# Kernel optimization log

Hardware: AMD Instinct MI355X
Metric: run time of the kernel (lower is better)

The kernel has to match this reference:

```python
import jax, jax.numpy as jnp
import numpy as np

EPS = 1.1920929e-07  # torch RMSNorm default eps = finfo(float32).eps

def rmsnorm(x, w):
    return x * jax.lax.rsqrt(jnp.mean(x * x, axis=-1, keepdims=True) + EPS) * w

def setup_inputs() -> dict:
    key = jax.random.key(0)
    ks = jax.random.split(key, 12)
    D, H, SC, ST = 1024, 16, 64, 16
    B, T = 2, 2048
    s = 0.02
    return {
        "x": jax.random.normal(ks[0], (B, T, D), jnp.float32),
        "qkv_w": jax.random.normal(ks[1], (3 * D, D), jnp.float32) * s,
        "o_w": jax.random.normal(ks[2], (D, D), jnp.float32) * s,
        "norm1_w": jnp.ones((D,), jnp.float32),
        "norm2_w": jnp.ones((D,), jnp.float32),
        "in_w": jax.random.normal(ks[3], (SC, D), jnp.float32) * s,
        "out_w": jax.random.normal(ks[4], (D, SC), jnp.float32) * s,  # zeros in torch init; randn for nontrivial baseline
        "A_log": jax.random.normal(ks[5], (SC, ST), jnp.float32) * 0.1,
        "Bp_w": jax.random.normal(ks[6], (ST, SC), jnp.float32) * s,
        "Cp_w": jax.random.normal(ks[7], (ST, SC), jnp.float32) * s,
        "dt_w": jax.random.normal(ks[8], (SC, SC), jnp.float32) * s,
        "dt_b": jnp.full((SC,), -3.0, jnp.float32),
        "gate_w": jax.random.normal(ks[9], (SC, D), jnp.float32) * s,
    }

def selective_scan(h, in_w, out_w, A_log, Bp_w, Cp_w, dt_w, dt_b, gate_w):
    B, T, D = h.shape
    SC, ST = A_log.shape
    z = h @ in_w.T                      # [B,T,SC]
    gate = jax.nn.silu(h @ gate_w.T)    # [B,T,SC]
    A = -jnp.exp(A_log)                 # [SC,ST]
    Bi = z @ Bp_w.T                     # [B,T,ST]
    Ci = z @ Cp_w.T                     # [B,T,ST]
    dt = jax.nn.softplus(z @ dt_w.T + dt_b)  # [B,T,SC]
    A_bar = 1.0 + dt[..., None] * A     # [B,T,SC,ST]

    def step(state, inp):
        a_bar, dtz_t, b_t, c_t = inp    # [B,SC,ST],[B,SC],[B,ST],[B,ST]
        state = a_bar * state + dtz_t[:, :, None] * b_t[:, None, :]
        y = jnp.sum(state * c_t[:, None, :], axis=-1)  # [B,SC]
        return state, y

    init = jnp.zeros((B, SC, ST), h.dtype)
    xs = (jnp.swapaxes(A_bar, 0, 1), jnp.swapaxes(dt * z, 0, 1),
          jnp.swapaxes(Bi, 0, 1), jnp.swapaxes(Ci, 0, 1))
    _, ys = jax.lax.scan(step, init, xs)      # [T,B,SC]
    y = jnp.swapaxes(ys, 0, 1) * gate         # [B,T,SC]
    return y @ out_w.T                        # [B,T,D]

def reference(x, qkv_w, o_w, norm1_w, norm2_w, in_w, out_w, A_log, Bp_w, Cp_w, dt_w, dt_b, gate_w):
    B, T, D = x.shape
    H = 16
    hd = D // H
    h = rmsnorm(x, norm1_w)
    qkv = (h @ qkv_w.T).reshape(B, T, 3, H, hd)
    qkv = jnp.transpose(qkv, (2, 0, 3, 1, 4))  # [3,B,H,T,hd]
    q, k, v = qkv[0], qkv[1], qkv[2]
    attn = jnp.einsum('bhqd,bhkd->bhqk', q, k) / np.sqrt(hd).astype(np.float32)
    mask = jnp.tril(jnp.ones((T, T), bool))
    attn = jnp.where(mask, attn, -jnp.inf)
    attn = jax.nn.softmax(attn, axis=-1)
    out = jnp.einsum('bhqk,bhkd->bhqd', attn, v)
    out = jnp.transpose(out, (0, 2, 1, 3)).reshape(B, T, D)
    x = x + out @ o_w.T
    h2 = rmsnorm(x, norm2_w)
    x = x + selective_scan(h2, in_w, out_w, A_log, Bp_w, Cp_w, dt_w, dt_b, gate_w)
    return x
```

## Files before the change

### kernel.cpp

```cpp
#include <hip/hip_runtime.h>
#include <hip/hip_bf16.h>
#include <math.h>

typedef __hip_bfloat16 bf16;
typedef __attribute__((ext_vector_type(4))) float v_f32x4;
typedef __attribute__((ext_vector_type(4))) unsigned short v_u16x4;
typedef __attribute__((ext_vector_type(8))) unsigned short v_u16x8;
typedef __attribute__((ext_vector_type(8))) __bf16 v_bf16x8;

#define NB 2
#define NT 2048
#define ND 1024
#define NH 16
#define NSC 64
#define NST 16
#define NM (NB*NT)
#define RMS_EPS 1.1920929e-07f
#define NCHUNK 32
#define CLEN 64

__device__ inline float b2f(unsigned short u) {
  union { unsigned int i; float f; } v; v.i = ((unsigned int)u) << 16; return v.f;
}
__device__ inline unsigned short f2b(float f) {
  union { float f; unsigned int i; } v; v.f = f;
  unsigned int r = (v.i + 0x7FFF + ((v.i >> 16) & 1)) >> 16;
  return (unsigned short)r;
}

__device__ inline void gl_lds16(const bf16* g, bf16* l) {
  __builtin_amdgcn_global_load_lds((__attribute__((address_space(1))) void*)g,
                                   (__attribute__((address_space(3))) void*)l,
                                   16, 0, 0);
}

__global__ __launch_bounds__(256) void cvt_all_kernel(
    const float* __restrict__ qkv_w, const float* __restrict__ o_w,
    const float* __restrict__ out_w, const float* __restrict__ in_w,
    const float* __restrict__ gate_w, const float* __restrict__ dt_w,
    const float* __restrict__ Bp_w, const float* __restrict__ Cp_w,
    bf16* __restrict__ qkvw_b, bf16* __restrict__ ow_b, bf16* __restrict__ outw_b,
    bf16* __restrict__ W1, bf16* __restrict__ W2) {
  const int blk = blockIdx.x, t = threadIdx.x;
  const float* src; bf16* dst; int base;
  if (blk < 3072)      { src = qkv_w;  dst = qkvw_b;      base = blk; }
  else if (blk < 4096) { src = o_w;    dst = ow_b;        base = blk - 3072; }
  else if (blk < 4160) { src = out_w;  dst = outw_b;      base = blk - 4096; }
  else if (blk < 4224) { src = in_w;   dst = W1;          base = blk - 4160; }
  else if (blk < 4288) { src = gate_w; dst = W1 + 65536;  base = blk - 4224; }
  else if (blk < 4292) { src = dt_w;   dst = W2;          base = blk - 4288; }
  else if (blk == 4292){ src = Bp_w;   dst = W2 + 4096;   base = 0; }
  else if (blk == 4293){ src = Cp_w;   dst = W2 + 5120;   base = 0; }
  else {
    v_u16x8 z;
    #pragma unroll
    for (int i = 0; i < 8; i++) z[i] = 0;
    *(v_u16x8*)(W2 + 6144 + t * 8) = z;
    return;
  }
  int i = base * 256 + t;
  v_f32x4 v = ((const v_f32x4*)src)[i];
  v_u16x4 o;
  o[0] = f2b(v[0]); o[1] = f2b(v[1]); o[2] = f2b(v[2]); o[3] = f2b(v[3]);
  ((v_u16x4*)dst)[i] = o;
}

__global__ __launch_bounds__(256) void rmsnorm_kernel(
    const float* __restrict__ x, const float* __restrict__ w, bf16* __restrict__ out) {
  const int row = blockIdx.x;
  const int t = threadIdx.x;
  v_f32x4 xv = *(const v_f32x4*)(x + (size_t)row * ND + t * 4);
  float s = xv[0]*xv[0] + xv[1]*xv[1] + xv[2]*xv[2] + xv[3]*xv[3];
  #pragma unroll
  for (int off = 32; off; off >>= 1) s += __shfl_xor(s, off, 64);
  __shared__ float red[4];
  __shared__ float scale_s;
  if ((t & 63) == 0) red[t >> 6] = s;
  __syncthreads();
  if (t == 0) {
    float tot = red[0] + red[1] + red[2] + red[3];
    scale_s = rsqrtf(tot * (1.0f / ND) + RMS_EPS);
  }
  __syncthreads();
  float sc = scale_s;
  v_f32x4 wv = *(const v_f32x4*)(w + t * 4);
  unsigned short* orow = (unsigned short*)out + (size_t)row * ND + t * 4;
  v_u16x4 o;
  o[0] = f2b(xv[0] * sc * wv[0]);
  o[1] = f2b(xv[1] * sc * wv[1]);
  o[2] = f2b(xv[2] * sc * wv[2]);
  o[3] = f2b(xv[3] * sc * wv[3]);
  *(v_u16x4*)orow = o;
}

template <bool RES, bool OUTF32>
__global__ __launch_bounds__(256) void gemm_bt_kernel(
    const bf16* __restrict__ A, const bf16* __restrict__ Bw,
    const float* __restrict__ res, void* __restrict__ Cout, int N, int K, int lda) {
  __shared__ alignas(16) bf16 As[128 * 32];
  __shared__ alignas(16) bf16 Bs[128 * 32];
  const int tid = threadIdx.x;
  const int wid = tid >> 6;
  const int lane = tid & 63;
  const int c = lane & 15;
  const int quad = lane >> 4;
  const int m0 = blockIdx.y * 128;
  const int n0 = blockIdx.x * 128;
  const int wm = (wid >> 1) * 64;
  const int wn = (wid & 1) * 64;
  const int srow = tid >> 2;
  const int schunk = tid & 3;

  const bf16* Ap0 = A + (size_t)(m0 + srow) * lda + schunk * 8;
  const bf16* Ap1 = Ap0 + (size_t)64 * lda;
  const bf16* Bp0 = Bw + (size_t)(n0 + srow) * K + schunk * 8;
  const bf16* Bp1 = Bp0 + (size_t)64 * K;
  bf16* AsW0 = As + wid * 512;
  bf16* AsW1 = As + 2048 + wid * 512;
  bf16* BsW0 = Bs + wid * 512;
  bf16* BsW1 = Bs + 2048 + wid * 512;

  v_f32x4 acc[4][4];
  #pragma unroll
  for (int i = 0; i < 4; i++)
    #pragma unroll
    for (int j = 0; j < 4; j++)
      #pragma unroll
      for (int r = 0; r < 4; r++) acc[i][j][r] = 0.0f;

  const int nk = K >> 5;
  for (int kt = 0; kt < nk; kt++) {
    gl_lds16(Ap0 + kt * 32, AsW0);
    gl_lds16(Ap1 + kt * 32, AsW1);
    gl_lds16(Bp0 + kt * 32, BsW0);
    gl_lds16(Bp1 + kt * 32, BsW1);
    __syncthreads();
    v_bf16x8 af[4], bfw[4];
    #pragma unroll
    for (int i = 0; i < 4; i++)
      af[i] = *(const v_bf16x8*)&As[(wm + i * 16 + c) * 32 + quad * 8];
    #pragma unroll
    for (int j = 0; j < 4; j++)
      bfw[j] = *(const v_bf16x8*)&Bs[(wn + j * 16 + c) * 32 + quad * 8];
    #pragma unroll
    for (int i = 0; i < 4; i++)
      #pragma unroll
      for (int j = 0; j < 4; j++)
        acc[i][j] = __builtin_amdgcn_mfma_f32_16x16x32_bf16(af[i], bfw[j], acc[i][j], 0, 0, 0);
    __syncthreads();
  }

  #pragma unroll
  for (int i = 0; i < 4; i++)
    #pragma unroll
    for (int j = 0; j < 4; j++)
      #pragma unroll
      for (int r = 0; r < 4; r++) {
        int rg = m0 + wm + i * 16 + quad * 4 + r;
        int cg = n0 + wn + j * 16 + c;
        size_t idx = (size_t)rg * N + cg;
        float v = acc[i][j][r];
        if (RES) v += res[idx];
        if (OUTF32) ((float*)Cout)[idx] = v;
        else ((bf16*)Cout)[idx] = __float2bfloat16(v);
      }
}

template <bool RES, bool OUTF32>
__global__ __launch_bounds__(256) void gemm_bt64_kernel(
    const bf16* __restrict__ A, const bf16* __restrict__ Bw,
    const float* __restrict__ res, void* __restrict__ Cout, int N, int K, int lda) {
  __shared__ alignas(16) bf16 As[64 * 32];
  __shared__ alignas(16) bf16 Bs[128 * 32];
  const int tid = threadIdx.x;
  const int wid = tid >> 6;
  const int lane = tid & 63;
  const int c = lane & 15;
  const int quad = lane >> 4;
  const int m0 = blockIdx.y * 64;
  const int n0 = blockIdx.x * 128;
  const int wm = (wid & 1) * 32;
  const int wn = (wid >> 1) * 64;
  const int srow = tid >> 2;
  const int schunk = tid & 3;

  const bf16* Ap = A + (size_t)(m0 + srow) * lda + schunk * 8;
  const bf16* Bp0 = Bw + (size_t)(n0 + srow) * K + schunk * 8;
  const bf16* Bp1 = Bp0 + (size_t)64 * K;
  bf16* AsW  = As + wid * 512;
  bf16* BsW0 = Bs + wid * 512;
  bf16* BsW1 = Bs + 2048 + wid * 512;

  v_f32x4 acc[2][4];
  #pragma unroll
  for (int i = 0; i < 2; i++)
    #pragma unroll
    for (int j = 0; j < 4; j++)
      #pragma unroll
      for (int r = 0; r < 4; r++) acc[i][j][r] = 0.0f;

  const int nk = K >> 5;
  for (int kt = 0; kt < nk; kt++) {
    gl_lds16(Ap + kt * 32, AsW);
    gl_lds16(Bp0 + kt * 32, BsW0);
    gl_lds16(Bp1 + kt * 32, BsW1);
    __syncthreads();
    v_bf16x8 af[2], bfw[4];
    #pragma unroll
    for (int i = 0; i < 2; i++)
      af[i] = *(const v_bf16x8*)&As[(wm + i * 16 + c) * 32 + quad * 8];
    #pragma unroll
    for (int j = 0; j < 4; j++)
      bfw[j] = *(const v_bf16x8*)&Bs[(wn + j * 16 + c) * 32 + quad * 8];
    #pragma unroll
    for (int i = 0; i < 2; i++)
      #pragma unroll
      for (int j = 0; j < 4; j++)
        acc[i][j] = __builtin_amdgcn_mfma_f32_16x16x32_bf16(af[i], bfw[j], acc[i][j], 0, 0, 0);
    __syncthreads();
  }

  #pragma unroll
  for (int i = 0; i < 2; i++)
    #pragma unroll
    for (int j = 0; j < 4; j++)
      #pragma unroll
      for (int r = 0; r < 4; r++) {
        int rg = m0 + wm + i * 16 + quad * 4 + r;
        int cg = n0 + wn + j * 16 + c;
        size_t idx = (size_t)rg * N + cg;
        float v = acc[i][j][r];
        if (RES) v += res[idx];
        if (OUTF32) ((float*)Cout)[idx] = v;
        else ((bf16*)Cout)[idx] = __float2bfloat16(v);
      }
}

template <bool OUTF32>
__global__ __launch_bounds__(256) void gemm_skinny_kernel(
    const bf16* __restrict__ A, const bf16* __restrict__ Bw,
    void* __restrict__ Cout, int K, int lda) {
  __shared__ alignas(16) bf16 As[16 * 32];
  __shared__ alignas(16) bf16 Bs[128 * 32];
  const int tid = threadIdx.x;
  const int w = tid >> 6;
  const int lane = tid & 63;
  const int c = lane & 15;
  const int quad = lane >> 4;
  const int m0 = blockIdx.x * 16;
  const int lrow = lane >> 2, lchunk = lane & 3;

  const bf16* ApL = A + (size_t)(m0 + lrow) * lda + lchunk * 8;
  const bf16* BpL0 = Bw + (size_t)(w * 16 + lrow) * K + lchunk * 8;
  const bf16* BpL1 = Bw + (size_t)(64 + w * 16 + lrow) * K + lchunk * 8;
  bf16* BsW0 = Bs + w * 512;
  bf16* BsW1 = Bs + 2048 + w * 512;

  v_f32x4 acc[2];
  #pragma unroll
  for (int j = 0; j < 2; j++)
    #pragma unroll
    for (int r = 0; r < 4; r++) acc[j][r] = 0.0f;

  const int nk = K >> 5;
  for (int kt = 0; kt < nk; kt++) {
    if (w == 0) gl_lds16(ApL + kt * 32, As);
    gl_lds16(BpL0 + kt * 32, BsW0);
    gl_lds16(BpL1 + kt * 32, BsW1);
    __syncthreads();
    v_bf16x8 af = *(const v_bf16x8*)&As[c * 32 + quad * 8];
    #pragma unroll
    for (int j = 0; j < 2; j++) {
      v_bf16x8 bfw = *(const v_bf16x8*)&Bs[(w * 32 + j * 16 + c) * 32 + quad * 8];
      acc[j] = __builtin_amdgcn_mfma_f32_16x16x32_bf16(af, bfw, acc[j], 0, 0, 0);
    }
    __syncthreads();
  }

  #pragma unroll
  for (int j = 0; j < 2; j++)
    #pragma unroll
    for (int r = 0; r < 4; r++) {
      size_t idx = (size_t)(m0 + quad * 4 + r) * 128 + w * 32 + j * 16 + c;
      if (OUTF32) ((float*)Cout)[idx] = acc[j][r];
      else ((bf16*)Cout)[idx] = __float2bfloat16(acc[j][r]);
    }
}

__global__ __launch_bounds__(256) void vtrans_kernel(const bf16* __restrict__ qkv,
                                                     bf16* __restrict__ VtG) {
  __shared__ alignas(16) bf16 Vs[64 * 72];
  const int tid = threadIdx.x;
  const int t0 = blockIdx.x * 64;
  const int bh = blockIdx.y;
  const int b = bh >> 4, h = bh & 15;
  const int srow = tid >> 2, schunk = tid & 3;
  {
    const bf16* src = qkv + (size_t)(b * NT + t0 + srow) * 3072 + 2048 + h * 64 + schunk * 16;
    *(v_u16x8*)&Vs[srow * 72 + schunk * 16] = *(const v_u16x8*)src;
    *(v_u16x8*)&Vs[srow * 72 + schunk * 16 + 8] = *(const v_u16x8*)(src + 8);
  }
  __syncthreads();
  const unsigned short* Vsu = (const unsigned short*)Vs;
  v_u16x8 a, bvec;
  #pragma unroll
  for (int i = 0; i < 8; i++) a[i] = Vsu[(schunk * 16 + i) * 72 + srow];
  #pragma unroll
  for (int i = 0; i < 8; i++) bvec[i] = Vsu[(schunk * 16 + 8 + i) * 72 + srow];
  bf16* dst = VtG + (size_t)(bh * 64 + srow) * NT + t0 + schunk * 16;
  *(v_u16x8*)dst = a;
  *(v_u16x8*)(dst + 8) = bvec;
}

__global__ __launch_bounds__(256) void attn_kernel(const bf16* __restrict__ qkv,
                                                   const bf16* __restrict__ VtG,
                                                   bf16* __restrict__ out) {
  __shared__ alignas(16) bf16 Qs[128 * 72];
  __shared__ alignas(16) bf16 Ks[64 * 72];
  __shared__ alignas(16) bf16 Vt[64 * 72];
  __shared__ alignas(16) bf16 Ps[128 * 72];
  const int tid = threadIdx.x;
  const int w = tid >> 6;
  const int lane = tid & 63;
  const int c = lane & 15;
  const int quad = lane >> 4;
  const int id = blockIdx.x;
  const int bh = id & 31;
  const int j5 = id >> 5;
  const int qt2 = (j5 & 8) ? (15 - (j5 & 7)) : (j5 & 7);
  const int b = bh >> 4;
  const int h = bh & 15;
  const int srow = tid >> 2;
  const int schunk = tid & 3;
  const int qbase = qt2 * 128;

  #pragma unroll
  for (int g = 0; g < 2; g++) {
    const bf16* src = qkv + (size_t)(b * NT + qbase + g * 64 + srow) * 3072 + h * 64 + schunk * 16;
    *(v_u16x8*)&Qs[(g * 64 + srow) * 72 + schunk * 16] = *(const v_u16x8*)src;
    *(v_u16x8*)&Qs[(g * 64 + srow) * 72 + schunk * 16 + 8] = *(const v_u16x8*)(src + 8);
  }
  __syncthreads();
  v_bf16x8 aq[2][2];
  #pragma unroll
  for (int g = 0; g < 2; g++) {
    aq[g][0] = *(const v_bf16x8*)&Qs[(g * 64 + w * 16 + c) * 72 + quad * 8];
    aq[g][1] = *(const v_bf16x8*)&Qs[(g * 64 + w * 16 + c) * 72 + 32 + quad * 8];
  }

  float l_part[2][4];
  v_f32x4 o[2][4];
  #pragma unroll
  for (int g = 0; g < 2; g++)
    #pragma unroll
    for (int r = 0; r < 4; r++) l_part[g][r] = 0.0f;
  #pragma unroll
  for (int g = 0; g < 2; g++)
    #pragma unroll
    for (int j = 0; j < 4; j++)
      #pragma unroll
      for (int r = 0; r < 4; r++) o[g][j][r] = 0.0f;

  const int ktmax = 2 * qt2 + 1;
  for (int kt = 0; kt <= ktmax; kt++) {
    {
      const bf16* ksrc = qkv + (size_t)(b * NT + kt * 64 + srow) * 3072 + 1024 + h * 64 + schunk * 16;
      *(v_u16x8*)&Ks[srow * 72 + schunk * 16] = *(const v_u16x8*)ksrc;
      *(v_u16x8*)&Ks[srow * 72 + schunk * 16 + 8] = *(const v_u16x8*)(ksrc + 8);
      const bf16* vsrc = VtG + (size_t)(bh * 64 + srow) * NT + kt * 64 + schunk * 16;
      *(v_u16x8*)&Vt[srow * 72 + schunk * 16] = *(const v_u16x8*)vsrc;
      *(v_u16x8*)&Vt[srow * 72 + schunk * 16 + 8] = *(const v_u16x8*)(vsrc + 8);
    }
    __syncthreads();

    #pragma unroll
    for (int g = 0; g < 2; g++) {
      const int ktd = 2 * qt2 + g;
      if (kt <= ktd) {
        const bool diag = (kt == ktd);
        #pragma unroll
        for (int j4 = 0; j4 < 4; j4++) {
          v_bf16x8 bk0 = *(const v_bf16x8*)&Ks[(j4 * 16 + c) * 72 + quad * 8];
          v_bf16x8 bk1 = *(const v_bf16x8*)&Ks[(j4 * 16 + c) * 72 + 32 + quad * 8];
          v_f32x4 z;
          #pragma unroll
          for (int r = 0; r < 4; r++) z[r] = 0.0f;
          z = __builtin_amdgcn_mfma_f32_16x16x32_bf16(aq[g][0], bk0, z, 0, 0, 0);
          z = __builtin_amdgcn_mfma_f32_16x16x32_bf16(aq[g][1], bk1, z, 0, 0, 0);
          #pragma unroll
          for (int r = 0; r < 4; r++) {
            float p = __expf(z[r] * 0.125f);
            if (diag && (j4 * 16 + c) > (w * 16 + quad * 4 + r)) p = 0.0f;
            l_part[g][r] += p;
            Ps[(g * 64 + w * 16 + quad * 4 + r) * 72 + j4 * 16 + c] = __float2bfloat16(p);
          }
        }
        #pragma unroll
        for (int ks = 0; ks < 2; ks++) {
          v_bf16x8 ap = *(const v_bf16x8*)&Ps[(g * 64 + w * 16 + c) * 72 + ks * 32 + quad * 8];
          #pragma unroll
          for (int jn = 0; jn < 4; jn++) {
            v_bf16x8 bv = *(const v_bf16x8*)&Vt[(jn * 16 + c) * 72 + ks * 32 + quad * 8];
            o[g][jn] = __builtin_amdgcn_mfma_f32_16x16x32_bf16(ap, bv, o[g][jn], 0, 0, 0);
          }
        }
      }
    }
    __syncthreads();
  }

  #pragma unroll
  for (int g = 0; g < 2; g++)
    #pragma unroll
    for (int r = 0; r < 4; r++) {
      float l = l_part[g][r];
      l += __shfl_xor(l, 1, 64);
      l += __shfl_xor(l, 2, 64);
      l += __shfl_xor(l, 4, 64);
      l += __shfl_xor(l, 8, 64);
      l_part[g][r] = l;
    }

  #pragma unroll
  for (int g = 0; g < 2; g++)
    #pragma unroll
    for (int jn = 0; jn < 4; jn++)
      #pragma unroll
      for (int r = 0; r < 4; r++) {
        int qg = qbase + g * 64 + w * 16 + quad * 4 + r;
        out[(size_t)(b * NT + qg) * ND + h * 64 + jn * 16 + c] =
            __float2bfloat16(o[g][jn][r] / l_part[g][r]);
      }
}

__global__ __launch_bounds__(256) void scanprep_kernel(
    const bf16* __restrict__ zg, const float* __restrict__ P2, const float* __restrict__ dt_b,
    float* __restrict__ dt_a, float* __restrict__ dtz_a, float* __restrict__ gate_a) {
  const int row = blockIdx.x * 4 + (threadIdx.x >> 6);
  const int c = threadIdx.x & 63;
  const unsigned short* zgu = (const unsigned short*)zg;
  float z = b2f(zgu[(size_t)row * 128 + c]);
  float g = b2f(zgu[(size_t)row * 128 + 64 + c]);
  float a = P2[(size_t)row * 128 + c] + dt_b[c];
  float dt = (a > 20.0f) ? a : log1pf(__expf(a));
  dt_a[(size_t)row * NSC + c] = dt;
  dtz_a[(size_t)row * NSC + c] = dt * z;
  gate_a[(size_t)row * NSC + c] = g / (1.0f + __expf(-g));
}

__global__ __launch_bounds__(256) void scanA_kernel(
    const float* __restrict__ dt_a, const float* __restrict__ dtz_a,
    const float* __restrict__ P2, const float* __restrict__ A_log,
    float* __restrict__ Pbuf, float* __restrict__ Sbuf) {
  __shared__ float dtS[CLEN * 16], dtzS[CLEN * 16], biS[CLEN * 16];
  const int k = blockIdx.x, scg = blockIdx.y, b = blockIdx.z;
  const int tid = threadIdx.x;
  const int t0 = k * CLEN;
  {
    int r = tid >> 2, c4 = (tid & 3) * 4;
    *(v_f32x4*)&dtS[r * 16 + c4]  = *(const v_f32x4*)&dt_a[(size_t)(b * NT + t0 + r) * NSC + scg * 16 + c4];
    *(v_f32x4*)&dtzS[r * 16 + c4] = *(const v_f32x4*)&dtz_a[(size_t)(b * NT + t0 + r) * NSC + scg * 16 + c4];
    *(v_f32x4*)&biS[r * 16 + c4]  = *(const v_f32x4*)&P2[(size_t)(b * NT + t0 + r) * 128 + 64 + c4];
  }
  __syncthreads();
  const int st = tid & 15, scl = tid >> 4;
  const float A = -__expf(A_log[(scg * 16 + scl) * NST + st]);
  float P = 1.0f, s = 0.0f;
  #pragma unroll
  for (int t = 0; t < CLEN; t++) {
    float a = fmaf(dtS[t * 16 + scl], A, 1.0f);
    float u = dtzS[t * 16 + scl] * biS[t * 16 + st];
    P *= a;
    s = fmaf(a, s, u);
  }
  size_t idx = (size_t)(b * NCHUNK + k) * 1024 + scg * 256 + tid;
  Pbuf[idx] = P;
  Sbuf[idx] = s;
}

__global__ __launch_bounds__(1024) void scanB_kernel(
    const float* __restrict__ Pbuf, const float* __restrict__ Sbuf,
    float* __restrict__ init) {
  const int b = blockIdx.x;
  const int tid = threadIdx.x;
  float P[NCHUNK], S[NCHUNK];
  #pragma unroll
  for (int kk = 0; kk < NCHUNK; kk++) {
    size_t idx = (size_t)(b * NCHUNK + kk) * 1024 + tid;
    P[kk] = Pbuf[idx];
    S[kk] = Sbuf[idx];
  }
  float s = 0.0f;
  #pragma unroll
  for (int kk = 0; kk < NCHUNK; kk++) {
    init[(size_t)(b * NCHUNK + kk) * 1024 + tid] = s;
    s = fmaf(P[kk], s, S[kk]);
  }
}

__global__ __launch_bounds__(256) void scanC_kernel(
    const float* __restrict__ dt_a, const float* __restrict__ dtz_a,
    const float* __restrict__ P2, const float* __restrict__ gate_a,
    const float* __restrict__ A_log, const float* __restrict__ init,
    bf16* __restrict__ ys) {
  __shared__ float dtS[CLEN * 16], dtzS[CLEN * 16], biS[CLEN * 16], ciS[CLEN * 16], gS[CLEN * 16];
  const int k = blockIdx.x, scg = blockIdx.y, b = blockIdx.z;
  const int tid = threadIdx.x;
  const int t0 = k * CLEN;
  {
    int r = tid >> 2, c4 = (tid & 3) * 4;
    *(v_f32x4*)&dtS[r * 16 + c4]  = *(const v_f32x4*)&dt_a[(size_t)(b * NT + t0 + r) * NSC + scg * 16 + c4];
    *(v_f32x4*)&dtzS[r * 16 + c4] = *(const v_f32x4*)&dtz_a[(size_t)(b * NT + t0 + r) * NSC + scg * 16 + c4];
    *(v_f32x4*)&biS[r * 16 + c4]  = *(const v_f32x4*)&P2[(size_t)(b * NT + t0 + r) * 128 + 64 + c4];
    *(v_f32x4*)&ciS[r * 16 + c4]  = *(const v_f32x4*)&P2[(size_t)(b * NT + t0 + r) * 128 + 80 + c4];
    *(v_f32x4*)&gS[r * 16 + c4]   = *(const v_f32x4*)&gate_a[(size_t)(b * NT + t0 + r) * NSC + scg * 16 + c4];
  }
  __syncthreads();
  const int st = tid & 15, scl = tid >> 4;
  const float A = -__expf(A_log[(scg * 16 + scl) * NST + st]);
  float s = init[(size_t)(b * NCHUNK + k) * 1024 + scg * 256 + tid];
  for (int t = 0; t < CLEN; t++) {
    float a = fmaf(dtS[t * 16 + scl], A, 1.0f);
    float u = dtzS[t * 16 + scl] * biS[t * 16 + st];
    s = fmaf(a, s, u);
    float pv = s * ciS[t * 16 + st];
    pv += __shfl_xor(pv, 1, 64);
    pv += __shfl_xor(pv, 2, 64);
    pv += __shfl_xor(pv, 4, 64);
    pv += __shfl_xor(pv, 8, 64);
    if (st == 0)
      ys[(size_t)(b * NT + t0 + t) * NSC + scg * 16 + scl] = __float2bfloat16(pv * gS[t * 16 + scl]);
  }
}

extern "C" void kernel_launch(void* const* d_in, const int* in_sizes, int n_in,
                              void* d_out, int out_size, void* d_ws, size_t ws_size,
                              hipStream_t stream) {
  const float* x      = (const float*)d_in[0];
  const float* qkv_w  = (const float*)d_in[1];
  const float* o_w    = (const float*)d_in[2];
  const float* n1w    = (const float*)d_in[3];
  const float* n2w    = (const float*)d_in[4];
  const float* in_w   = (const float*)d_in[5];
  const float* out_w  = (const float*)d_in[6];
  const float* A_log  = (const float*)d_in[7];
  const float* Bp_w   = (const float*)d_in[8];
  const float* Cp_w   = (const float*)d_in[9];
  const float* dt_w   = (const float*)d_in[10];
  const float* dt_b   = (const float*)d_in[11];
  const float* gate_w = (const float*)d_in[12];
  float* out = (float*)d_out;

  char* ws = (char*)d_ws;
  size_t off = 0;
  auto alloc = [&](size_t bytes) {
    char* p = ws + off;
    off += (bytes + 255) & ~(size_t)255;
    return p;
  };
  bf16* qkvw_b = (bf16*)alloc((size_t)3 * ND * ND * 2);
  bf16* ow_b   = (bf16*)alloc((size_t)ND * ND * 2);
  bf16* outw_b = (bf16*)alloc((size_t)ND * NSC * 2);
  bf16* W1     = (bf16*)alloc((size_t)128 * ND * 2);
  bf16* W2     = (bf16*)alloc((size_t)128 * NSC * 2);
  char* region0 = alloc((size_t)NM * 3 * ND * 2);
  char* region1 = alloc((size_t)NM * ND * 2);
  bf16* VtG    = (bf16*)alloc((size_t)NB * NH * 64 * NT * 2);
  bf16*  zg    = (bf16*)alloc((size_t)NM * 128 * 2);
  float* P2    = (float*)alloc((size_t)NM * 128 * 4);
  float* dt_a  = (float*)alloc((size_t)NM * NSC * 4);
  float* dtz_a = (float*)alloc((size_t)NM * NSC * 4);
  float* gate_a= (float*)alloc((size_t)NM * NSC * 4);
  bf16*  ys    = (bf16*)alloc((size_t)NM * NSC * 2);
  float* Pbuf  = (float*)alloc((size_t)NB * NCHUNK * 1024 * 4);
  float* Sbuf  = (float*)alloc((size_t)NB * NCHUNK * 1024 * 4);
  float* initb = (float*)alloc((size_t)NB * NCHUNK * 1024 * 4);

  bf16*  qkv     = (bf16*)region0;
  float* x1      = (float*)region0;
  bf16*  h       = (bf16*)region1;
  bf16*  attnout = (bf16*)region1;
  bf16*  h2      = (bf16*)region1;

  cvt_all_kernel<<<4295, 256, 0, stream>>>(qkv_w, o_w, out_w, in_w, gate_w, dt_w,
                                           Bp_w, Cp_w, qkvw_b, ow_b, outw_b, W1, W2);
  rmsnorm_kernel<<<NM, 256, 0, stream>>>(x, n1w, h);
  gemm_bt_kernel<false, false><<<dim3(3 * ND / 128, NM / 128), 256, 0, stream>>>(
      h, qkvw_b, nullptr, (void*)qkv, 3 * ND, ND, ND);
  vtrans_kernel<<<dim3(NT / 64, NB * NH), 256, 0, stream>>>(qkv, VtG);
  attn_kernel<<<(NT / 128) * NB * NH, 256, 0, stream>>>(qkv, VtG, attnout);
  gemm_bt64_kernel<true, true><<<dim3(ND / 128, NM / 64), 256, 0, stream>>>(
      attnout, ow_b, x, (void*)x1, ND, ND, ND);
  rmsnorm_kernel<<<NM, 256, 0, stream>>>(x1, n2w, h2);
  gemm_skinny_kernel<false><<<NM / 16, 256, 0, stream>>>(h2, W1, (void*)zg, ND, ND);
  gemm_skinny_kernel<true><<<NM / 16, 256, 0, stream>>>(zg, W2, (void*)P2, NSC, 128);
  scanprep_kernel<<<NM / 4, 256, 0, stream>>>(zg, P2, dt_b, dt_a, dtz_a, gate_a);
  scanA_kernel<<<dim3(NCHUNK, 4, NB), 256, 0, stream>>>(dt_a, dtz_a, P2, A_log, Pbuf, Sbuf);
  scanB_kernel<<<NB, 1024, 0, stream>>>(Pbuf, Sbuf, initb);
  scanC_kernel<<<dim3(NCHUNK, 4, NB), 256, 0, stream>>>(dt_a, dtz_a, P2, gate_a, A_log, initb, ys);
  gemm_bt64_kernel<true, true><<<dim3(ND / 128, NM / 64), 256, 0, stream>>>(
      ys, outw_b, x1, (void*)out, ND, NSC, NSC);
}
```

Before: 300.3 us.

## Fuse pre-attention and SSM-projection kernels, shrink attention tile, inline chunk-carry scan

Merges the weight conversion and first RMSNorm into one launch. Fuses the second RMSNorm, both skinny projection GEMMs and the scan-prep elementwise step into a single kernel that keeps intermediates in LDS. Attention moves from 128-row to 64-row query tiles with a reordered tile mapping, doubling the block count. The separate chunk-carry scan kernel is removed, so each scanC block recomputes its initial state serially from Pbuf and Sbuf. Together these cut launches and global round-trips, at the cost of redundant carry work and fewer query rows per K/V tile load in attention.

```diff
diff --git a/kernel.cpp b/kernel.cpp
--- a/kernel.cpp
+++ b/kernel.cpp
@@ -34,14 +34,37 @@
                                    16, 0, 0);
 }
 
-__global__ __launch_bounds__(256) void cvt_all_kernel(
+__global__ __launch_bounds__(256) void cvt_rms_kernel(
     const float* __restrict__ qkv_w, const float* __restrict__ o_w,
     const float* __restrict__ out_w, const float* __restrict__ in_w,
     const float* __restrict__ gate_w, const float* __restrict__ dt_w,
     const float* __restrict__ Bp_w, const float* __restrict__ Cp_w,
     bf16* __restrict__ qkvw_b, bf16* __restrict__ ow_b, bf16* __restrict__ outw_b,
-    bf16* __restrict__ W1, bf16* __restrict__ W2) {
+    bf16* __restrict__ W1, bf16* __restrict__ W2,
+    const float* __restrict__ x, const float* __restrict__ n1w, bf16* __restrict__ h) {
   const int blk = blockIdx.x, t = threadIdx.x;
+  if (blk >= 4295) {
+    const int row = blk - 4295;
+    v_f32x4 xv = *(const v_f32x4*)(x + (size_t)row * ND + t * 4);
+    float s = xv[0]*xv[0] + xv[1]*xv[1] + xv[2]*xv[2] + xv[3]*xv[3];
+    #pragma unroll
+    for (int off = 32; off; off >>= 1) s += __shfl_xor(s, off, 64);
+    __shared__ float red[4];
+    __shared__ float scale_s;
+    if ((t & 63) == 0) red[t >> 6] = s;
+    __syncthreads();
+    if (t == 0) scale_s = rsqrtf((red[0] + red[1] + red[2] + red[3]) * (1.0f / ND) + RMS_EPS);
+    __syncthreads();
+    float sc = scale_s;
+    v_f32x4 wv = *(const v_f32x4*)(n1w + t * 4);
+    v_u16x4 o;
+    o[0] = f2b(xv[0] * sc * wv[0]);
+    o[1] = f2b(xv[1] * sc * wv[1]);
+    o[2] = f2b(xv[2] * sc * wv[2]);
+    o[3] = f2b(xv[3] * sc * wv[3]);
+    *(v_u16x4*)((unsigned short*)h + (size_t)row * ND + t * 4) = o;
+    return;
+  }
   const float* src; bf16* dst; int base;
   if (blk < 3072)      { src = qkv_w;  dst = qkvw_b;      base = blk; }
   else if (blk < 4096) { src = o_w;    dst = ow_b;        base = blk - 3072; }
@@ -65,34 +88,6 @@
   ((v_u16x4*)dst)[i] = o;
 }
 
-__global__ __launch_bounds__(256) void rmsnorm_kernel(
-    const float* __restrict__ x, const float* __restrict__ w, bf16* __restrict__ out) {
-  const int row = blockIdx.x;
-  const int t = threadIdx.x;
-  v_f32x4 xv = *(const v_f32x4*)(x + (size_t)row * ND + t * 4);
-  float s = xv[0]*xv[0] + xv[1]*xv[1] + xv[2]*xv[2] + xv[3]*xv[3];
-  #pragma unroll
-  for (int off = 32; off; off >>= 1) s += __shfl_xor(s, off, 64);
-  __shared__ float red[4];
-  __shared__ float scale_s;
-  if ((t & 63) == 0) red[t >> 6] = s;
-  __syncthreads();
-  if (t == 0) {
-    float tot = red[0] + red[1] + red[2] + red[3];
-    scale_s = rsqrtf(tot * (1.0f / ND) + RMS_EPS);
-  }
-  __syncthreads();
-  float sc = scale_s;
-  v_f32x4 wv = *(const v_f32x4*)(w + t * 4);
-  unsigned short* orow = (unsigned short*)out + (size_t)row * ND + t * 4;
-  v_u16x4 o;
-  o[0] = f2b(xv[0] * sc * wv[0]);
-  o[1] = f2b(xv[1] * sc * wv[1]);
-  o[2] = f2b(xv[2] * sc * wv[2]);
-  o[3] = f2b(xv[3] * sc * wv[3]);
-  *(v_u16x4*)orow = o;
-}
-
 template <bool RES, bool OUTF32>
 __global__ __launch_bounds__(256) void gemm_bt_kernel(
     const bf16* __restrict__ A, const bf16* __restrict__ Bw,
@@ -236,57 +231,6 @@
       }
 }
 
-template <bool OUTF32>
-__global__ __launch_bounds__(256) void gemm_skinny_kernel(
-    const bf16* __restrict__ A, const bf16* __restrict__ Bw,
-    void* __restrict__ Cout, int K, int lda) {
-  __shared__ alignas(16) bf16 As[16 * 32];
-  __shared__ alignas(16) bf16 Bs[128 * 32];
-  const int tid = threadIdx.x;
-  const int w = tid >> 6;
-  const int lane = tid & 63;
-  const int c = lane & 15;
-  const int quad = lane >> 4;
-  const int m0 = blockIdx.x * 16;
-  const int lrow = lane >> 2, lchunk = lane & 3;
-
-  const bf16* ApL = A + (size_t)(m0 + lrow) * lda + lchunk * 8;
-  const bf16* BpL0 = Bw + (size_t)(w * 16 + lrow) * K + lchunk * 8;
-  const bf16* BpL1 = Bw + (size_t)(64 + w * 16 + lrow) * K + lchunk * 8;
-  bf16* BsW0 = Bs + w * 512;
-  bf16* BsW1 = Bs + 2048 + w * 512;
-
-  v_f32x4 acc[2];
-  #pragma unroll
-  for (int j = 0; j < 2; j++)
-    #pragma unroll
-    for (int r = 0; r < 4; r++) acc[j][r] = 0.0f;
-
-  const int nk = K >> 5;
-  for (int kt = 0; kt < nk; kt++) {
-    if (w == 0) gl_lds16(ApL + kt * 32, As);
-    gl_lds16(BpL0 + kt * 32, BsW0);
-    gl_lds16(BpL1 + kt * 32, BsW1);
-    __syncthreads();
-    v_bf16x8 af = *(const v_bf16x8*)&As[c * 32 + quad * 8];
-    #pragma unroll
-    for (int j = 0; j < 2; j++) {
-      v_bf16x8 bfw = *(const v_bf16x8*)&Bs[(w * 32 + j * 16 + c) * 32 + quad * 8];
-      acc[j] = __builtin_amdgcn_mfma_f32_16x16x32_bf16(af, bfw, acc[j], 0, 0, 0);
-    }
-    __syncthreads();
-  }
-
-  #pragma unroll
-  for (int j = 0; j < 2; j++)
-    #pragma unroll
-    for (int r = 0; r < 4; r++) {
-      size_t idx = (size_t)(m0 + quad * 4 + r) * 128 + w * 32 + j * 16 + c;
-      if (OUTF32) ((float*)Cout)[idx] = acc[j][r];
-      else ((bf16*)Cout)[idx] = __float2bfloat16(acc[j][r]);
-    }
-}
-
 __global__ __launch_bounds__(256) void vtrans_kernel(const bf16* __restrict__ qkv,
                                                      bf16* __restrict__ VtG) {
   __shared__ alignas(16) bf16 Vs[64 * 72];
@@ -315,10 +259,10 @@
 __global__ __launch_bounds__(256) void attn_kernel(const bf16* __restrict__ qkv,
                                                    const bf16* __restrict__ VtG,
                                                    bf16* __restrict__ out) {
-  __shared__ alignas(16) bf16 Qs[128 * 72];
+  __shared__ alignas(16) bf16 Qs[64 * 72];
   __shared__ alignas(16) bf16 Ks[64 * 72];
   __shared__ alignas(16) bf16 Vt[64 * 72];
-  __shared__ alignas(16) bf16 Ps[128 * 72];
+  __shared__ alignas(16) bf16 Ps[64 * 72];
   const int tid = threadIdx.x;
   const int w = tid >> 6;
   const int lane = tid & 63;
@@ -327,42 +271,32 @@
   const int id = blockIdx.x;
   const int bh = id & 31;
   const int j5 = id >> 5;
-  const int qt2 = (j5 & 8) ? (15 - (j5 & 7)) : (j5 & 7);
+  const int j0 = j5 & 7;
+  const int qt = (j5 & 24) | (((j5 >> 3) & 1) ? (7 - j0) : j0);
   const int b = bh >> 4;
   const int h = bh & 15;
   const int srow = tid >> 2;
   const int schunk = tid & 3;
-  const int qbase = qt2 * 128;
-
-  #pragma unroll
-  for (int g = 0; g < 2; g++) {
-    const bf16* src = qkv + (size_t)(b * NT + qbase + g * 64 + srow) * 3072 + h * 64 + schunk * 16;
-    *(v_u16x8*)&Qs[(g * 64 + srow) * 72 + schunk * 16] = *(const v_u16x8*)src;
-    *(v_u16x8*)&Qs[(g * 64 + srow) * 72 + schunk * 16 + 8] = *(const v_u16x8*)(src + 8);
+
+  {
+    const bf16* src = qkv + (size_t)(b * NT + qt * 64 + srow) * 3072 + h * 64 + schunk * 16;
+    *(v_u16x8*)&Qs[srow * 72 + schunk * 16] = *(const v_u16x8*)src;
+    *(v_u16x8*)&Qs[srow * 72 + schunk * 16 + 8] = *(const v_u16x8*)(src + 8);
   }
   __syncthreads();
-  v_bf16x8 aq[2][2];
-  #pragma unroll
-  for (int g = 0; g < 2; g++) {
-    aq[g][0] = *(const v_bf16x8*)&Qs[(g * 64 + w * 16 + c) * 72 + quad * 8];
-    aq[g][1] = *(const v_bf16x8*)&Qs[(g * 64 + w * 16 + c) * 72 + 32 + quad * 8];
-  }
-
-  float l_part[2][4];
-  v_f32x4 o[2][4];
-  #pragma unroll
-  for (int g = 0; g < 2; g++)
-    #pragma unroll
-    for (int r = 0; r < 4; r++) l_part[g][r] = 0.0f;
-  #pragma unroll
-  for (int g = 0; g < 2; g++)
-    #pragma unroll
-    for (int j = 0; j < 4; j++)
-      #pragma unroll
-      for (int r = 0; r < 4; r++) o[g][j][r] = 0.0f;
-
-  const int ktmax = 2 * qt2 + 1;
-  for (int kt = 0; kt <= ktmax; kt++) {
+  v_bf16x8 aq0 = *(const v_bf16x8*)&Qs[(w * 16 + c) * 72 + quad * 8];
+  v_bf16x8 aq1 = *(const v_bf16x8*)&Qs[(w * 16 + c) * 72 + 32 + quad * 8];
+
+  float l_part[4];
+  v_f32x4 o[4];
+  #pragma unroll
+  for (int r = 0; r < 4; r++) l_part[r] = 0.0f;
+  #pragma unroll
+  for (int j = 0; j < 4; j++)
+    #pragma unroll
+    for (int r = 0; r < 4; r++) o[j][r] = 0.0f;
+
+  for (int kt = 0; kt <= qt; kt++) {
     {
       const bf16* ksrc = qkv + (size_t)(b * NT + kt * 64 + srow) * 3072 + 1024 + h * 64 + schunk * 16;
       *(v_u16x8*)&Ks[srow * 72 + schunk * 16] = *(const v_u16x8*)ksrc;
@@ -373,79 +307,162 @@
     }
     __syncthreads();
 
-    #pragma unroll
-    for (int g = 0; g < 2; g++) {
-      const int ktd = 2 * qt2 + g;
-      if (kt <= ktd) {
-        const bool diag = (kt == ktd);
-        #pragma unroll
-        for (int j4 = 0; j4 < 4; j4++) {
-          v_bf16x8 bk0 = *(const v_bf16x8*)&Ks[(j4 * 16 + c) * 72 + quad * 8];
-          v_bf16x8 bk1 = *(const v_bf16x8*)&Ks[(j4 * 16 + c) * 72 + 32 + quad * 8];
-          v_f32x4 z;
-          #pragma unroll
-          for (int r = 0; r < 4; r++) z[r] = 0.0f;
-          z = __builtin_amdgcn_mfma_f32_16x16x32_bf16(aq[g][0], bk0, z, 0, 0, 0);
-          z = __builtin_amdgcn_mfma_f32_16x16x32_bf16(aq[g][1], bk1, z, 0, 0, 0);
-          #pragma unroll
-          for (int r = 0; r < 4; r++) {
-            float p = __expf(z[r] * 0.125f);
-            if (diag && (j4 * 16 + c) > (w * 16 + quad * 4 + r)) p = 0.0f;
-            l_part[g][r] += p;
-            Ps[(g * 64 + w * 16 + quad * 4 + r) * 72 + j4 * 16 + c] = __float2bfloat16(p);
-          }
-        }
-        #pragma unroll
-        for (int ks = 0; ks < 2; ks++) {
-          v_bf16x8 ap = *(const v_bf16x8*)&Ps[(g * 64 + w * 16 + c) * 72 + ks * 32 + quad * 8];
-          #pragma unroll
-          for (int jn = 0; jn < 4; jn++) {
-            v_bf16x8 bv = *(const v_bf16x8*)&Vt[(jn * 16 + c) * 72 + ks * 32 + quad * 8];
-            o[g][jn] = __builtin_amdgcn_mfma_f32_16x16x32_bf16(ap, bv, o[g][jn], 0, 0, 0);
-          }
-        }
+    const bool diag = (kt == qt);
+    #pragma unroll
+    for (int j = 0; j < 4; j++) {
+      v_bf16x8 bk0 = *(const v_bf16x8*)&Ks[(j * 16 + c) * 72 + quad * 8];
+      v_bf16x8 bk1 = *(const v_bf16x8*)&Ks[(j * 16 + c) * 72 + 32 + quad * 8];
+      v_f32x4 z;
+      #pragma unroll
+      for (int r = 0; r < 4; r++) z[r] = 0.0f;
+      z = __builtin_amdgcn_mfma_f32_16x16x32_bf16(aq0, bk0, z, 0, 0, 0);
+      z = __builtin_amdgcn_mfma_f32_16x16x32_bf16(aq1, bk1, z, 0, 0, 0);
+      #pragma unroll
+      for (int r = 0; r < 4; r++) {
+        float p = __expf(z[r] * 0.125f);
+        if (diag && (j * 16 + c) > (w * 16 + quad * 4 + r)) p = 0.0f;
+        l_part[r] += p;
+        Ps[(w * 16 + quad * 4 + r) * 72 + j * 16 + c] = __float2bfloat16(p);
       }
     }
-    __syncthreads();
-  }
-
-  #pragma unroll
-  for (int g = 0; g < 2; g++)
+    #pragma unroll
+    for (int ks = 0; ks < 2; ks++) {
+      v_bf16x8 ap = *(const v_bf16x8*)&Ps[(w * 16 + c) * 72 + ks * 32 + quad * 8];
+      #pragma unroll
+      for (int jn = 0; jn < 4; jn++) {
+        v_bf16x8 bv = *(const v_bf16x8*)&Vt[(jn * 16 + c) * 72 + ks * 32 + quad * 8];
+        o[jn] = __builtin_amdgcn_mfma_f32_16x16x32_bf16(ap, bv, o[jn], 0, 0, 0);
+      }
+    }
+    __syncthreads();
+  }
+
+  #pragma unroll
+  for (int r = 0; r < 4; r++) {
+    float l = l_part[r];
+    l += __shfl_xor(l, 1, 64);
+    l += __shfl_xor(l, 2, 64);
+    l += __shfl_xor(l, 4, 64);
+    l += __shfl_xor(l, 8, 64);
+    l_part[r] = l;
+  }
+
+  #pragma unroll
+  for (int jn = 0; jn < 4; jn++)
     #pragma unroll
     for (int r = 0; r < 4; r++) {
-      float l = l_part[g][r];
-      l += __shfl_xor(l, 1, 64);
-      l += __shfl_xor(l, 2, 64);
-      l += __shfl_xor(l, 4, 64);
-      l += __shfl_xor(l, 8, 64);
-      l_part[g][r] = l;
-    }
-
-  #pragma unroll
-  for (int g = 0; g < 2; g++)
-    #pragma unroll
-    for (int jn = 0; jn < 4; jn++)
-      #pragma unroll
-      for (int r = 0; r < 4; r++) {
-        int qg = qbase + g * 64 + w * 16 + quad * 4 + r;
-        out[(size_t)(b * NT + qg) * ND + h * 64 + jn * 16 + c] =
-            __float2bfloat16(o[g][jn][r] / l_part[g][r]);
+      int qg = qt * 64 + w * 16 + quad * 4 + r;
+      out[(size_t)(b * NT + qg) * ND + h * 64 + jn * 16 + c] =
+          __float2bfloat16(o[jn][r] / l_part[r]);
+    }
+}
+
+__global__ __launch_bounds__(256) void proj_scan_kernel(
+    const float* __restrict__ x1, const float* __restrict__ n2w,
+    const bf16* __restrict__ W1, const bf16* __restrict__ W2,
+    const float* __restrict__ dt_b,
+    float* __restrict__ dt_a, float* __restrict__ dtz_a,
+    float* __restrict__ gate_a, float* __restrict__ P2) {
+  __shared__ alignas(16) bf16 h2S[16 * 1032];
+  __shared__ alignas(16) bf16 Bs[128 * 32];
+  __shared__ alignas(16) bf16 zgS[16 * 136];
+  const int tid = threadIdx.x;
+  const int w = tid >> 6, lane = tid & 63, c = lane & 15, quad = lane >> 4;
+  const int m0 = blockIdx.x * 16;
+  unsigned short* h2Su = (unsigned short*)h2S;
+  unsigned short* zgSu = (unsigned short*)zgS;
+
+  {
+    const int r16 = tid >> 4, ct = tid & 15;
+    const float* xr = x1 + (size_t)(m0 + r16) * ND + ct * 64;
+    v_f32x4 xv[16];
+    float ss = 0.0f;
+    #pragma unroll
+    for (int i = 0; i < 16; i++) {
+      xv[i] = *(const v_f32x4*)(xr + i * 4);
+      ss += xv[i][0]*xv[i][0] + xv[i][1]*xv[i][1] + xv[i][2]*xv[i][2] + xv[i][3]*xv[i][3];
+    }
+    ss += __shfl_xor(ss, 1, 64);
+    ss += __shfl_xor(ss, 2, 64);
+    ss += __shfl_xor(ss, 4, 64);
+    ss += __shfl_xor(ss, 8, 64);
+    float sc = rsqrtf(ss * (1.0f / ND) + RMS_EPS);
+    const float* wr = n2w + ct * 64;
+    #pragma unroll
+    for (int i = 0; i < 16; i++) {
+      v_f32x4 wv = *(const v_f32x4*)(wr + i * 4);
+      v_u16x4 o;
+      o[0] = f2b(xv[i][0] * sc * wv[0]);
+      o[1] = f2b(xv[i][1] * sc * wv[1]);
+      o[2] = f2b(xv[i][2] * sc * wv[2]);
+      o[3] = f2b(xv[i][3] * sc * wv[3]);
+      *(v_u16x4*)&h2Su[r16 * 1032 + ct * 64 + i * 4] = o;
+    }
+  }
+  __syncthreads();
+
+  const int lrow = lane >> 2, lk = lane & 3;
+  v_f32x4 acc[2];
+  #pragma unroll
+  for (int j = 0; j < 2; j++)
+    #pragma unroll
+    for (int r = 0; r < 4; r++) acc[j][r] = 0.0f;
+  for (int kt = 0; kt < 32; kt++) {
+    gl_lds16(W1 + (size_t)(w * 32 + lrow) * 1024 + kt * 32 + lk * 8, Bs + (w * 32) * 32);
+    gl_lds16(W1 + (size_t)(w * 32 + 16 + lrow) * 1024 + kt * 32 + lk * 8, Bs + (w * 32 + 16) * 32);
+    __syncthreads();
+    v_bf16x8 af = *(const v_bf16x8*)&h2S[c * 1032 + kt * 32 + quad * 8];
+    #pragma unroll
+    for (int j = 0; j < 2; j++) {
+      v_bf16x8 bfw = *(const v_bf16x8*)&Bs[(w * 32 + j * 16 + c) * 32 + quad * 8];
+      acc[j] = __builtin_amdgcn_mfma_f32_16x16x32_bf16(af, bfw, acc[j], 0, 0, 0);
+    }
+    __syncthreads();
+  }
+  #pragma unroll
+  for (int j = 0; j < 2; j++)
+    #pragma unroll
+    for (int r = 0; r < 4; r++)
+      zgSu[(quad * 4 + r) * 136 + w * 32 + j * 16 + c] = f2b(acc[j][r]);
+  __syncthreads();
+
+  v_f32x4 acc2[2];
+  #pragma unroll
+  for (int j = 0; j < 2; j++)
+    #pragma unroll
+    for (int r = 0; r < 4; r++) acc2[j][r] = 0.0f;
+  for (int kt = 0; kt < 2; kt++) {
+    gl_lds16(W2 + (size_t)(w * 32 + lrow) * 64 + kt * 32 + lk * 8, Bs + (w * 32) * 32);
+    gl_lds16(W2 + (size_t)(w * 32 + 16 + lrow) * 64 + kt * 32 + lk * 8, Bs + (w * 32 + 16) * 32);
+    __syncthreads();
+    v_bf16x8 af = *(const v_bf16x8*)&zgS[c * 136 + kt * 32 + quad * 8];
+    #pragma unroll
+    for (int j = 0; j < 2; j++) {
+      v_bf16x8 bfw = *(const v_bf16x8*)&Bs[(w * 32 + j * 16 + c) * 32 + quad * 8];
+      acc2[j] = __builtin_amdgcn_mfma_f32_16x16x32_bf16(af, bfw, acc2[j], 0, 0, 0);
+    }
+    __syncthreads();
+  }
+
+  #pragma unroll
+  for (int j = 0; j < 2; j++)
+    #pragma unroll
+    for (int r = 0; r < 4; r++) {
+      const int row = quad * 4 + r;
+      const int col = w * 32 + j * 16 + c;
+      const size_t grow = (size_t)(m0 + row);
+      if (w < 2) {
+        float z = b2f(zgSu[row * 136 + col]);
+        float a = acc2[j][r] + dt_b[col];
+        float dt = (a > 20.0f) ? a : log1pf(__expf(a));
+        dt_a[grow * NSC + col] = dt;
+        dtz_a[grow * NSC + col] = dt * z;
+      } else {
+        P2[grow * 128 + col] = acc2[j][r];
+        float g = b2f(zgSu[row * 136 + col]);
+        gate_a[grow * NSC + (col - 64)] = g / (1.0f + __expf(-g));
       }
-}
-
-__global__ __launch_bounds__(256) void scanprep_kernel(
-    const bf16* __restrict__ zg, const float* __restrict__ P2, const float* __restrict__ dt_b,
-    float* __restrict__ dt_a, float* __restrict__ dtz_a, float* __restrict__ gate_a) {
-  const int row = blockIdx.x * 4 + (threadIdx.x >> 6);
-  const int c = threadIdx.x & 63;
-  const unsigned short* zgu = (const unsigned short*)zg;
-  float z = b2f(zgu[(size_t)row * 128 + c]);
-  float g = b2f(zgu[(size_t)row * 128 + 64 + c]);
-  float a = P2[(size_t)row * 128 + c] + dt_b[c];
-  float dt = (a > 20.0f) ? a : log1pf(__expf(a));
-  dt_a[(size_t)row * NSC + c] = dt;
-  dtz_a[(size_t)row * NSC + c] = dt * z;
-  gate_a[(size_t)row * NSC + c] = g / (1.0f + __expf(-g));
+    }
 }
 
 __global__ __launch_bounds__(256) void scanA_kernel(
@@ -478,31 +495,11 @@
   Sbuf[idx] = s;
 }
 
-__global__ __launch_bounds__(1024) void scanB_kernel(
-    const float* __restrict__ Pbuf, const float* __restrict__ Sbuf,
-    float* __restrict__ init) {
-  const int b = blockIdx.x;
-  const int tid = threadIdx.x;
-  float P[NCHUNK], S[NCHUNK];
-  #pragma unroll
-  for (int kk = 0; kk < NCHUNK; kk++) {
-    size_t idx = (size_t)(b * NCHUNK + kk) * 1024 + tid;
-    P[kk] = Pbuf[idx];
-    S[kk] = Sbuf[idx];
-  }
-  float s = 0.0f;
-  #pragma unroll
-  for (int kk = 0; kk < NCHUNK; kk++) {
-    init[(size_t)(b * NCHUNK + kk) * 1024 + tid] = s;
-    s = fmaf(P[kk], s, S[kk]);
-  }
-}
-
 __global__ __launch_bounds__(256) void scanC_kernel(
     const float* __restrict__ dt_a, const float* __restrict__ dtz_a,
     const float* __restrict__ P2, const float* __restrict__ gate_a,
-    const float* __restrict__ A_log, const float* __restrict__ init,
-    bf16* __restrict__ ys) {
+    const float* __restrict__ A_log, const float* __restrict__ Pbuf,
+    const float* __restrict__ Sbuf, bf16* __restrict__ ys) {
   __shared__ float dtS[CLEN * 16], dtzS[CLEN * 16], biS[CLEN * 16], ciS[CLEN * 16], gS[CLEN * 16];
   const int k = blockIdx.x, scg = blockIdx.y, b = blockIdx.z;
   const int tid = threadIdx.x;
@@ -515,10 +512,14 @@
     *(v_f32x4*)&ciS[r * 16 + c4]  = *(const v_f32x4*)&P2[(size_t)(b * NT + t0 + r) * 128 + 80 + c4];
     *(v_f32x4*)&gS[r * 16 + c4]   = *(const v_f32x4*)&gate_a[(size_t)(b * NT + t0 + r) * NSC + scg * 16 + c4];
   }
-  __syncthreads();
   const int st = tid & 15, scl = tid >> 4;
   const float A = -__expf(A_log[(scg * 16 + scl) * NST + st]);
-  float s = init[(size_t)(b * NCHUNK + k) * 1024 + scg * 256 + tid];
+  float s = 0.0f;
+  for (int kk = 0; kk < k; kk++) {
+    size_t idx = (size_t)(b * NCHUNK + kk) * 1024 + scg * 256 + tid;
+    s = fmaf(Pbuf[idx], s, Sbuf[idx]);
+  }
+  __syncthreads();
   for (int t = 0; t < CLEN; t++) {
     float a = fmaf(dtS[t * 16 + scl], A, 1.0f);
     float u = dtzS[t * 16 + scl] * biS[t * 16 + st];
@@ -566,7 +567,6 @@
   char* region0 = alloc((size_t)NM * 3 * ND * 2);
   char* region1 = alloc((size_t)NM * ND * 2);
   bf16* VtG    = (bf16*)alloc((size_t)NB * NH * 64 * NT * 2);
-  bf16*  zg    = (bf16*)alloc((size_t)NM * 128 * 2);
   float* P2    = (float*)alloc((size_t)NM * 128 * 4);
   float* dt_a  = (float*)alloc((size_t)NM * NSC * 4);
   float* dtz_a = (float*)alloc((size_t)NM * NSC * 4);
@@ -574,30 +574,26 @@
   bf16*  ys    = (bf16*)alloc((size_t)NM * NSC * 2);
   float* Pbuf  = (float*)alloc((size_t)NB * NCHUNK * 1024 * 4);
   float* Sbuf  = (float*)alloc((size_t)NB * NCHUNK * 1024 * 4);
-  float* initb = (float*)alloc((size_t)NB * NCHUNK * 1024 * 4);
 
   bf16*  qkv     = (bf16*)region0;
   float* x1      = (float*)region0;
   bf16*  h       = (bf16*)region1;
   bf16*  attnout = (bf16*)region1;
-  bf16*  h2      = (bf16*)region1;
-
-  cvt_all_kernel<<<4295, 256, 0, stream>>>(qkv_w, o_w, out_w, in_w, gate_w, dt_w,
-                                           Bp_w, Cp_w, qkvw_b, ow_b, outw_b, W1, W2);
-  rmsnorm_kernel<<<NM, 256, 0, stream>>>(x, n1w, h);
+
+  cvt_rms_kernel<<<4295 + NM, 256, 0, stream>>>(qkv_w, o_w, out_w, in_w, gate_w, dt_w,
+                                                Bp_w, Cp_w, qkvw_b, ow_b, outw_b, W1, W2,
+                                                x, n1w, h);
   gemm_bt_kernel<false, false><<<dim3(3 * ND / 128, NM / 128), 256, 0, stream>>>(
       h, qkvw_b, nullptr, (void*)qkv, 3 * ND, ND, ND);
   vtrans_kernel<<<dim3(NT / 64, NB * NH), 256, 0, stream>>>(qkv, VtG);
-  attn_kernel<<<(NT / 128) * NB * NH, 256, 0, stream>>>(qkv, VtG, attnout);
+  attn_kernel<<<(NT / 64) * NB * NH, 256, 0, stream>>>(qkv, VtG, attnout);
   gemm_bt64_kernel<true, true><<<dim3(ND / 128, NM / 64), 256, 0, stream>>>(
       attnout, ow_b, x, (void*)x1, ND, ND, ND);
-  rmsnorm_kernel<<<NM, 256, 0, stream>>>(x1, n2w, h2);
-  gemm_skinny_kernel<false><<<NM / 16, 256, 0, stream>>>(h2, W1, (void*)zg, ND, ND);
-  gemm_skinny_kernel<true><<<NM / 16, 256, 0, stream>>>(zg, W2, (void*)P2, NSC, 128);
-  scanprep_kernel<<<NM / 4, 256, 0, stream>>>(zg, P2, dt_b, dt_a, dtz_a, gate_a);
+  proj_scan_kernel<<<NM / 16, 256, 0, stream>>>(x1, n2w, W1, W2, dt_b,
+                                                dt_a, dtz_a, gate_a, P2);
   scanA_kernel<<<dim3(NCHUNK, 4, NB), 256, 0, stream>>>(dt_a, dtz_a, P2, A_log, Pbuf, Sbuf);
-  scanB_kernel<<<NB, 1024, 0, stream>>>(Pbuf, Sbuf, initb);
-  scanC_kernel<<<dim3(NCHUNK, 4, NB), 256, 0, stream>>>(dt_a, dtz_a, P2, gate_a, A_log, initb, ys);
+  scanC_kernel<<<dim3(NCHUNK, 4, NB), 256, 0, stream>>>(dt_a, dtz_a, P2, gate_a, A_log,
+                                                        Pbuf, Sbuf, ys);
   gemm_bt64_kernel<true, true><<<dim3(ND / 128, NM / 64), 256, 0, stream>>>(
       ys, outw_b, x1, (void*)out, ND, NSC, NSC);
 }
```

Result: faster. 270.6 us (-9.9%).
